# Kernel tuning notes

Measured on AMD Instinct MI355X. Metric: run time of the kernel, lower is better.

Reference implementation:

```python
import jax, jax.numpy as jnp
import numpy as np

N = 50000
IN, HID, OUT, HEADS = 128, 64, 64, 4


def seg_softmax(logits, seg, num):
    # softmax over edges grouped by destination node; logits [E, H]
    m = jax.ops.segment_max(logits, seg, num_segments=num)
    e = jnp.exp(logits - m[seg])
    s = jax.ops.segment_sum(e, seg, num_segments=num)
    return e / (s[seg] + 1e-16)


def gat_conv(x, src, dst, W, a_s, a_d, b, heads, concat):
    n = x.shape[0]
    h = (x @ W.T).reshape(n, heads, -1)           # [N, H, C]
    alpha_src = jnp.einsum('nhc,hc->nh', h, a_s)   # per-node src score
    alpha_dst = jnp.einsum('nhc,hc->nh', h, a_d)
    logits = jax.nn.leaky_relu(alpha_src[src] + alpha_dst[dst], 0.2)  # [E, H]
    alpha = seg_softmax(logits, dst, n)
    out = jax.ops.segment_sum(alpha[:, :, None] * h[src], dst, num_segments=n)  # [N, H, C]
    out = out.reshape(n, -1) if concat else out.mean(axis=1)
    return out + b


def setup_inputs():
    key = jax.random.key(0)
    ks = jax.random.split(key, 16)
    x = jax.random.normal(ks[0], (N, IN), dtype=jnp.float32)
    edge_index = jax.random.randint(ks[1], (2, 800000), 0, N, dtype=jnp.int64)

    def glorot(k, shape):
        fan = shape[-1]
        return jax.random.normal(k, shape, dtype=jnp.float32) / jnp.sqrt(jnp.float32(fan))

    d = {"x": x, "edge_index": edge_index}
    # layer 1: IN -> HID, HEADS heads, concat
    d["W1"] = glorot(ks[2], (HEADS * HID, IN))
    d["as1"] = glorot(ks[3], (HEADS, HID))
    d["ad1"] = glorot(ks[4], (HEADS, HID))
    d["b1"] = jnp.zeros((HEADS * HID,), jnp.float32)
    # layer 2: HID*HEADS -> HID, HEADS heads, concat
    d["W2"] = glorot(ks[5], (HEADS * HID, HEADS * HID))
    d["as2"] = glorot(ks[6], (HEADS, HID))
    d["ad2"] = glorot(ks[7], (HEADS, HID))
    d["b2"] = jnp.zeros((HEADS * HID,), jnp.float32)
    # layer 3: HID*HEADS -> OUT, 1 head
    d["W3"] = glorot(ks[8], (OUT, HEADS * HID))
    d["as3"] = glorot(ks[9], (1, OUT))
    d["ad3"] = glorot(ks[10], (1, OUT))
    d["b3"] = jnp.zeros((OUT,), jnp.float32)
    return d


def reference(x, edge_index, W1, as1, ad1, b1, W2, as2, ad2, b2, W3, as3, ad3, b3):
    # PyG GATConv adds self-loops by default
    loops = jnp.arange(N, dtype=edge_index.dtype)
    src = jnp.concatenate([edge_index[0], loops])
    dst = jnp.concatenate([edge_index[1], loops])

    h = jax.nn.relu(gat_conv(x, src, dst, W1, as1, ad1, b1, HEADS, True))
    h = jax.nn.relu(gat_conv(h, src, dst, W2, as2, ad2, b2, HEADS, True))
    out = gat_conv(h, src, dst, W3, as3, ad3, b3, 1, True)
    return out
```

## Files before the change

### kernel.cpp

```cpp
#include <hip/hip_runtime.h>
#include <hip/hip_bf16.h>
#include <math.h>


typedef __bf16 bf16x8 __attribute__((ext_vector_type(8)));
typedef float f32x4 __attribute__((ext_vector_type(4)));

#define QINV 2048.0f
#define QDQ  4.8828125e-4f

__device__ __forceinline__ void gload_lds16(const void* g, void* l) {
  __builtin_amdgcn_global_load_lds(
      (const __attribute__((address_space(1))) unsigned int*)g,
      (__attribute__((address_space(3))) unsigned int*)l, 16, 0, 0);
}

__device__ __forceinline__ unsigned int splitf(float a) {
  __hip_bfloat16 h = __float2bfloat16(a);
  float hf = __bfloat162float(h);
  __hip_bfloat16 l = __float2bfloat16(a - hf);
  return (unsigned int)__builtin_bit_cast(unsigned short, h) |
         ((unsigned int)__builtin_bit_cast(unsigned short, l) << 16);
}

__device__ __forceinline__ float leaky02(float l) {
  return (l >= 0.f) ? l : 0.2f * l;
}

__device__ __forceinline__ short quant16(float v) {
  int q = (int)rintf(v * QINV);
  q = q > 32767 ? 32767 : (q < -32768 ? -32768 : q);
  return (short)q;
}


__global__ void init_counts_kernel(int* counts, int n) {
  int i = blockIdx.x * blockDim.x + threadIdx.x;
  if (i < n) counts[i] = 1;
}

__global__ void hist_kernel(const int* __restrict__ dst, int e, int* counts) {
  int i = blockIdx.x * blockDim.x + threadIdx.x;
  if (i < e) atomicAdd(&counts[dst[i]], 1);
}

__global__ __launch_bounds__(1024) void block_sum_kernel(const int* __restrict__ counts,
                                                         int* __restrict__ bsum, int n) {
  __shared__ int red[1024];
  int i = blockIdx.x * 1024 + threadIdx.x;
  red[threadIdx.x] = (i < n) ? counts[i] : 0;
  __syncthreads();
  #pragma unroll
  for (int off = 512; off > 0; off >>= 1) {
    if (threadIdx.x < off) red[threadIdx.x] += red[threadIdx.x + off];
    __syncthreads();
  }
  if (threadIdx.x == 0) bsum[blockIdx.x] = red[0];
}

__global__ void scan_sums_kernel(int* bsum, int nb) {
  int t = threadIdx.x;
  int c = (t < nb) ? bsum[t] : 0;
  int v = c;
  #pragma unroll
  for (int off = 1; off < 64; off <<= 1) {
    int u = __shfl_up(v, off);
    if (t >= off) v += u;
  }
  if (t < nb) bsum[t] = v - c;
}

__global__ __launch_bounds__(1024) void scan_final_kernel(const int* __restrict__ counts,
    const int* __restrict__ bsum, int* __restrict__ offsets, int* __restrict__ cursor, int n) {
  __shared__ int sc[1024];
  int i = blockIdx.x * 1024 + threadIdx.x;
  int c = (i < n) ? counts[i] : 0;
  sc[threadIdx.x] = c;
  __syncthreads();
  for (int off = 1; off < 1024; off <<= 1) {
    int v = 0;
    if (threadIdx.x >= off) v = sc[threadIdx.x - off];
    __syncthreads();
    sc[threadIdx.x] += v;
    __syncthreads();
  }
  int excl = sc[threadIdx.x] - c + bsum[blockIdx.x];
  if (i < n) {
    offsets[i] = excl;
    cursor[i] = excl;
  } else if (i == n) {
    offsets[n] = excl;
  }
}

__global__ void scatter_kernel(const int* __restrict__ src, const int* __restrict__ dst,
                               int e800, int etot, int* cursor, int* __restrict__ ssrc) {
  int i = blockIdx.x * blockDim.x + threadIdx.x;
  if (i >= etot) return;
  int s, d;
  if (i < e800) { s = src[i]; d = dst[i]; }
  else          { s = i - e800; d = s; }
  int pos = atomicAdd(&cursor[d], 1);
  ssrc[pos] = s;
}

__global__ void split_kernel(const float* __restrict__ in, uint4* __restrict__ out, int count4) {
  int i = blockIdx.x * blockDim.x + threadIdx.x;
  if (i >= count4) return;
  float4 v = reinterpret_cast<const float4*>(in)[i];
  uint4 o;
  o.x = splitf(v.x); o.y = splitf(v.y); o.z = splitf(v.z); o.w = splitf(v.w);
  out[i] = o;
}

template <int KP, int BN, int WAVES_M, int WAVES_N>
__global__ __launch_bounds__(256) void gemm2_kernel(
    const unsigned short* __restrict__ A, const unsigned short* __restrict__ B,
    short* __restrict__ Cq, int M) {
  constexpr int BM = 64, BK = 64;
  constexpr int NK = KP / BK;
  constexpr int MFRAG = BM / WAVES_M / 16;
  constexpr int NFRAG = BN / WAVES_N / 16;
  __shared__ unsigned short As[2][BM * BK];
  __shared__ unsigned short Bs[2][BN * BK];

  const int tid = threadIdx.x;
  const int lane = tid & 63;
  const int wid = tid >> 6;
  const int m0 = blockIdx.x * BM;

  const int srow = tid >> 3;
  const int scolb = (tid & 7) * 16;
  const int sswz = (srow & 7) << 4;
  const char* aSrc = (const char*)A + (size_t)(m0 + srow) * (KP * 2) + (scolb ^ sswz);
  const char* bSrc = (const char*)B + (size_t)srow * (KP * 2) + (scolb ^ sswz);
  char* aDst0 = (char*)&As[0][0] + wid * 1024;
  char* bDst0 = (char*)&Bs[0][0] + wid * 1024;

  auto stage = [&](int buf, int kt) {
    const size_t ko = (size_t)kt * 128;
    char* ad = aDst0 + buf * (BM * 128);
    #pragma unroll
    for (int i = 0; i < BM / 32; ++i)
      gload_lds16(aSrc + ko + (size_t)i * 32 * (KP * 2), ad + i * 4096);
    char* bd = bDst0 + buf * (BN * 128);
    #pragma unroll
    for (int j = 0; j < BN / 32; ++j)
      gload_lds16(bSrc + ko + (size_t)j * 32 * (KP * 2), bd + j * 4096);
  };

  const int fr = lane & 15;
  const int fg = lane >> 4;
  const int fswz = (fr & 7) << 4;
  const int wm0 = (WAVES_M > 1) ? wid * (BM / WAVES_M) : 0;
  const int wn0 = (WAVES_N > 1) ? wid * (BN / WAVES_N) : 0;

  f32x4 acc[MFRAG][NFRAG];
  #pragma unroll
  for (int mi = 0; mi < MFRAG; ++mi)
    #pragma unroll
    for (int ni = 0; ni < NFRAG; ++ni) acc[mi][ni] = (f32x4)0.f;

  stage(0, 0);
  __syncthreads();

  for (int kt = 0; kt < NK; ++kt) {
    const int buf = kt & 1;
    if (kt + 1 < NK) stage(buf ^ 1, kt + 1);
    const char* asB = (const char*)&As[buf][0] + (wm0 + fr) * 128;
    const char* bsB = (const char*)&Bs[buf][0] + (wn0 + fr) * 128;
    #pragma unroll
    for (int kh = 0; kh < 2; ++kh) {
      const int kb = (kh * 64 + fg * 16) ^ fswz;
      bf16x8 af[MFRAG], bfr[NFRAG];
      #pragma unroll
      for (int mi = 0; mi < MFRAG; ++mi)
        af[mi] = *reinterpret_cast<const bf16x8*>(asB + mi * 16 * 128 + kb);
      #pragma unroll
      for (int ni = 0; ni < NFRAG; ++ni)
        bfr[ni] = *reinterpret_cast<const bf16x8*>(bsB + ni * 16 * 128 + kb);
      #pragma unroll
      for (int mi = 0; mi < MFRAG; ++mi)
        #pragma unroll
        for (int ni = 0; ni < NFRAG; ++ni)
          acc[mi][ni] = __builtin_amdgcn_mfma_f32_16x16x32_bf16(af[mi], bfr[ni], acc[mi][ni], 0, 0, 0);
    }
    __syncthreads();
  }

  #pragma unroll
  for (int mi = 0; mi < MFRAG; ++mi) {
    #pragma unroll
    for (int r = 0; r < 4; ++r) {
      int row = m0 + wm0 + mi * 16 + fg * 4 + r;
      if (row < M) {
        #pragma unroll
        for (int ni = 0; ni < NFRAG; ++ni)
          Cq[(size_t)row * BN + wn0 + ni * 16 + fr] = quant16(acc[mi][ni][r]);
      }
    }
  }
}

__global__ __launch_bounds__(256) void alpha4_kernel(const short* __restrict__ hq,
    const float* __restrict__ a_s, const float* __restrict__ a_d,
    float* __restrict__ asrc, float* __restrict__ adst, int n) {
  int wid = threadIdx.x >> 6;
  int lane = threadIdx.x & 63;
  int node = blockIdx.x * 4 + wid;
  if (node >= n) return;
  short4 q = *reinterpret_cast<const short4*>(&hq[(size_t)node * 256 + lane * 4]);
  float4 sv = *reinterpret_cast<const float4*>(&a_s[lane * 4]);
  float4 dv = *reinterpret_cast<const float4*>(&a_d[lane * 4]);
  float h0 = (float)q.x, h1 = (float)q.y, h2 = (float)q.z, h3 = (float)q.w;
  float ps = h0 * sv.x + h1 * sv.y + h2 * sv.z + h3 * sv.w;
  float pd = h0 * dv.x + h1 * dv.y + h2 * dv.z + h3 * dv.w;
  #pragma unroll
  for (int off = 1; off < 16; off <<= 1) {
    ps += __shfl_xor(ps, off);
    pd += __shfl_xor(pd, off);
  }
  if ((lane & 15) == 0) {
    int head = lane >> 4;
    asrc[node * 4 + head] = ps * QDQ;
    adst[node * 4 + head] = pd * QDQ;
  }
}

__global__ __launch_bounds__(256) void alpha1_kernel(const short* __restrict__ hq,
    const float* __restrict__ a_s, const float* __restrict__ a_d,
    float* __restrict__ asrc, float* __restrict__ adst, int n) {
  int wid = threadIdx.x >> 6;
  int lane = threadIdx.x & 63;
  int node = blockIdx.x * 4 + wid;
  if (node >= n) return;
  float hv = (float)hq[(size_t)node * 64 + lane];
  float ps = hv * a_s[lane];
  float pd = hv * a_d[lane];
  #pragma unroll
  for (int off = 1; off < 64; off <<= 1) {
    ps += __shfl_xor(ps, off);
    pd += __shfl_xor(pd, off);
  }
  if (lane == 0) { asrc[node] = ps * QDQ; adst[node] = pd * QDQ; }
}

template <bool RELU, bool SPLIT>
__global__ __launch_bounds__(256) void aggregate4_kernel(
    const short* __restrict__ hq, const float* __restrict__ asrc,
    const float* __restrict__ adst, const float* __restrict__ bias,
    const int* __restrict__ offsets, const int* __restrict__ ssrc,
    void* __restrict__ outp, int n) {
  int wid = threadIdx.x >> 6;
  int lane = threadIdx.x & 63;
  int node = blockIdx.x * 4 + wid;
  if (node >= n) return;
  int head = lane >> 4;
  float adv = adst[(size_t)node * 4 + head];
  int beg = offsets[node], end = offsets[node + 1];

  float m0 = -INFINITY, m1 = -INFINITY, m2 = -INFINITY, m3 = -INFINITY;
  int e = beg;
  for (; e + 3 < end; e += 4) {
    float l0 = leaky02(asrc[(size_t)ssrc[e + 0] * 4 + head] + adv);
    float l1 = leaky02(asrc[(size_t)ssrc[e + 1] * 4 + head] + adv);
    float l2 = leaky02(asrc[(size_t)ssrc[e + 2] * 4 + head] + adv);
    float l3 = leaky02(asrc[(size_t)ssrc[e + 3] * 4 + head] + adv);
    m0 = fmaxf(m0, l0); m1 = fmaxf(m1, l1);
    m2 = fmaxf(m2, l2); m3 = fmaxf(m3, l3);
  }
  for (; e < end; ++e)
    m0 = fmaxf(m0, leaky02(asrc[(size_t)ssrc[e] * 4 + head] + adv));
  const float m = fmaxf(fmaxf(m0, m1), fmaxf(m2, m3));

  float s0 = 0.f, s1 = 0.f, s2 = 0.f, s3 = 0.f;
  float4 A0 = {0, 0, 0, 0}, A1 = {0, 0, 0, 0}, A2 = {0, 0, 0, 0}, A3 = {0, 0, 0, 0};
  e = beg;
  for (; e + 3 < end; e += 4) {
    int c0 = ssrc[e + 0], c1 = ssrc[e + 1], c2 = ssrc[e + 2], c3 = ssrc[e + 3];
    float p0 = __expf(leaky02(asrc[(size_t)c0 * 4 + head] + adv) - m);
    float p1 = __expf(leaky02(asrc[(size_t)c1 * 4 + head] + adv) - m);
    float p2 = __expf(leaky02(asrc[(size_t)c2 * 4 + head] + adv) - m);
    float p3 = __expf(leaky02(asrc[(size_t)c3 * 4 + head] + adv) - m);
    short4 q0 = *reinterpret_cast<const short4*>(&hq[(size_t)c0 * 256 + lane * 4]);
    short4 q1 = *reinterpret_cast<const short4*>(&hq[(size_t)c1 * 256 + lane * 4]);
    short4 q2 = *reinterpret_cast<const short4*>(&hq[(size_t)c2 * 256 + lane * 4]);
    short4 q3 = *reinterpret_cast<const short4*>(&hq[(size_t)c3 * 256 + lane * 4]);
    s0 += p0; s1 += p1; s2 += p2; s3 += p3;
    A0.x += p0 * (float)q0.x; A0.y += p0 * (float)q0.y; A0.z += p0 * (float)q0.z; A0.w += p0 * (float)q0.w;
    A1.x += p1 * (float)q1.x; A1.y += p1 * (float)q1.y; A1.z += p1 * (float)q1.z; A1.w += p1 * (float)q1.w;
    A2.x += p2 * (float)q2.x; A2.y += p2 * (float)q2.y; A2.z += p2 * (float)q2.z; A2.w += p2 * (float)q2.w;
    A3.x += p3 * (float)q3.x; A3.y += p3 * (float)q3.y; A3.z += p3 * (float)q3.z; A3.w += p3 * (float)q3.w;
  }
  for (; e < end; ++e) {
    int c0 = ssrc[e];
    float p0 = __expf(leaky02(asrc[(size_t)c0 * 4 + head] + adv) - m);
    short4 q0 = *reinterpret_cast<const short4*>(&hq[(size_t)c0 * 256 + lane * 4]);
    s0 += p0;
    A0.x += p0 * (float)q0.x; A0.y += p0 * (float)q0.y; A0.z += p0 * (float)q0.z; A0.w += p0 * (float)q0.w;
  }
  float s = (s0 + s1) + (s2 + s3);
  float4 A;
  A.x = (A0.x + A1.x) + (A2.x + A3.x);
  A.y = (A0.y + A1.y) + (A2.y + A3.y);
  A.z = (A0.z + A1.z) + (A2.z + A3.z);
  A.w = (A0.w + A1.w) + (A2.w + A3.w);

  float inv = QDQ / (s + 1e-16f);
  float4 bv = *reinterpret_cast<const float4*>(&bias[lane * 4]);
  float4 o;
  o.x = A.x * inv + bv.x;
  o.y = A.y * inv + bv.y;
  o.z = A.z * inv + bv.z;
  o.w = A.w * inv + bv.w;
  if (RELU) {
    o.x = fmaxf(o.x, 0.f); o.y = fmaxf(o.y, 0.f);
    o.z = fmaxf(o.z, 0.f); o.w = fmaxf(o.w, 0.f);
  }
  if (SPLIT) {
    uint4 pk;
    pk.x = splitf(o.x); pk.y = splitf(o.y); pk.z = splitf(o.z); pk.w = splitf(o.w);
    reinterpret_cast<uint4*>(outp)[(size_t)node * 64 + lane] = pk;
  } else {
    reinterpret_cast<float4*>(outp)[(size_t)node * 64 + lane] = o;
  }
}

__global__ __launch_bounds__(256) void aggregate1_kernel(
    const short* __restrict__ hq, const float* __restrict__ asrc,
    const float* __restrict__ adst, const float* __restrict__ bias,
    const int* __restrict__ offsets, const int* __restrict__ ssrc,
    float* __restrict__ out, int n) {
  int wid = threadIdx.x >> 6;
  int lane = threadIdx.x & 63;
  int node = blockIdx.x * 4 + wid;
  if (node >= n) return;
  int g = lane >> 4;
  int w = lane & 15;
  float adv = adst[node];
  int beg = offsets[node], end = offsets[node + 1];

  float m = -INFINITY;
  for (int e = beg + lane; e < end; e += 64)
    m = fmaxf(m, leaky02(asrc[ssrc[e]] + adv));
  #pragma unroll
  for (int off = 1; off < 64; off <<= 1) m = fmaxf(m, __shfl_xor(m, off));

  float s = 0.f;
  float4 A = {0, 0, 0, 0};
  int e0 = beg;
  for (; e0 + 3 < end; e0 += 4) {
    int src = ssrc[e0 + g];
    float p = __expf(leaky02(asrc[src] + adv) - m);
    short4 q = *reinterpret_cast<const short4*>(&hq[(size_t)src * 64 + w * 4]);
    s += p;
    A.x += p * (float)q.x; A.y += p * (float)q.y;
    A.z += p * (float)q.z; A.w += p * (float)q.w;
  }
  if (e0 + g < end) {
    int src = ssrc[e0 + g];
    float p = __expf(leaky02(asrc[src] + adv) - m);
    short4 q = *reinterpret_cast<const short4*>(&hq[(size_t)src * 64 + w * 4]);
    s += p;
    A.x += p * (float)q.x; A.y += p * (float)q.y;
    A.z += p * (float)q.z; A.w += p * (float)q.w;
  }
  #pragma unroll
  for (int off = 16; off < 64; off <<= 1) {
    s += __shfl_xor(s, off);
    A.x += __shfl_xor(A.x, off);
    A.y += __shfl_xor(A.y, off);
    A.z += __shfl_xor(A.z, off);
    A.w += __shfl_xor(A.w, off);
  }
  if (g == 0) {
    float inv = QDQ / (s + 1e-16f);
    float4 bv = *reinterpret_cast<const float4*>(&bias[w * 4]);
    float4 o;
    o.x = A.x * inv + bv.x;
    o.y = A.y * inv + bv.y;
    o.z = A.z * inv + bv.z;
    o.w = A.w * inv + bv.w;
    *reinterpret_cast<float4*>(&out[(size_t)node * 64 + w * 4]) = o;
  }
}


extern "C" void kernel_launch(void* const* d_in, const int* in_sizes, int n_in,
                              void* d_out, int out_size, void* d_ws, size_t ws_size,
                              hipStream_t stream) {
  const float* x   = (const float*)d_in[0];
  const int*   ei  = (const int*)d_in[1];
  const float* W1  = (const float*)d_in[2];
  const float* as1 = (const float*)d_in[3];
  const float* ad1 = (const float*)d_in[4];
  const float* b1  = (const float*)d_in[5];
  const float* W2  = (const float*)d_in[6];
  const float* as2 = (const float*)d_in[7];
  const float* ad2 = (const float*)d_in[8];
  const float* b2  = (const float*)d_in[9];
  const float* W3  = (const float*)d_in[10];
  const float* as3 = (const float*)d_in[11];
  const float* ad3 = (const float*)d_in[12];
  const float* b3  = (const float*)d_in[13];
  float* out = (float*)d_out;

  const int n    = in_sizes[0] / 128;
  const int e800 = in_sizes[1] / 2;
  const int etot = e800 + n;
  const int Mpad = 50048;

  char* ws = (char*)d_ws;
  size_t off = 0;
  auto alloc = [&](size_t bytes) -> void* {
    void* p = ws + off;
    off = (off + bytes + 255) & ~(size_t)255;
    return p;
  };
  short*          featQ  = (short*)alloc((size_t)Mpad * 256 * 2);
  unsigned short* hsplit = (unsigned short*)alloc((size_t)Mpad * 512 * 2);
  unsigned short* w1s    = (unsigned short*)alloc((size_t)256 * 256 * 2);
  unsigned short* w2s    = (unsigned short*)alloc((size_t)256 * 512 * 2);
  unsigned short* w3s    = (unsigned short*)alloc((size_t)64 * 512 * 2);
  float* asrc    = (float*)alloc((size_t)n * 4 * 4);
  float* adst    = (float*)alloc((size_t)n * 4 * 4);
  int*   ssrc    = (int*)alloc((size_t)etot * 4);
  int*   offsets = (int*)alloc((size_t)(n + 1) * 4);
  int*   cursor  = (int*)alloc((size_t)n * 4);
  int*   counts  = (int*)alloc((size_t)n * 4);
  int*   bsum    = (int*)alloc((size_t)64 * 4);

  const int* esrc = ei;
  const int* edst = ei + e800;
  const int nbScan = (n + 1024) / 1024;

  init_counts_kernel<<<(n + 255) / 256, 256, 0, stream>>>(counts, n);
  hist_kernel<<<(e800 + 255) / 256, 256, 0, stream>>>(edst, e800, counts);
  block_sum_kernel<<<nbScan, 1024, 0, stream>>>(counts, bsum, n);
  scan_sums_kernel<<<1, 64, 0, stream>>>(bsum, nbScan);
  scan_final_kernel<<<nbScan, 1024, 0, stream>>>(counts, bsum, offsets, cursor, n);
  scatter_kernel<<<(etot + 255) / 256, 256, 0, stream>>>(esrc, edst, e800, etot, cursor, ssrc);

  split_kernel<<<(n * 128 / 4 + 255) / 256, 256, 0, stream>>>(x, (uint4*)hsplit, n * 128 / 4);
  split_kernel<<<(256 * 128 / 4 + 255) / 256, 256, 0, stream>>>(W1, (uint4*)w1s, 256 * 128 / 4);
  split_kernel<<<(256 * 256 / 4 + 255) / 256, 256, 0, stream>>>(W2, (uint4*)w2s, 256 * 256 / 4);
  split_kernel<<<(64 * 256 / 4 + 255) / 256, 256, 0, stream>>>(W3, (uint4*)w3s, 64 * 256 / 4);

  const int nodeBlocks = (n + 3) / 4;
  const int mBlocks = Mpad / 64;

  gemm2_kernel<256, 256, 1, 4><<<mBlocks, 256, 0, stream>>>(hsplit, w1s, featQ, n);
  alpha4_kernel<<<nodeBlocks, 256, 0, stream>>>(featQ, as1, ad1, asrc, adst, n);
  aggregate4_kernel<true, true><<<nodeBlocks, 256, 0, stream>>>(featQ, asrc, adst, b1, offsets, ssrc, hsplit, n);

  gemm2_kernel<512, 256, 1, 4><<<mBlocks, 256, 0, stream>>>(hsplit, w2s, featQ, n);
  alpha4_kernel<<<nodeBlocks, 256, 0, stream>>>(featQ, as2, ad2, asrc, adst, n);
  aggregate4_kernel<true, true><<<nodeBlocks, 256, 0, stream>>>(featQ, asrc, adst, b2, offsets, ssrc, hsplit, n);

  gemm2_kernel<512, 64, 4, 1><<<mBlocks, 256, 0, stream>>>(hsplit, w3s, featQ, n);
  alpha1_kernel<<<nodeBlocks, 256, 0, stream>>>(featQ, as3, ad3, asrc, adst, n);
  aggregate1_kernel<<<nodeBlocks, 256, 0, stream>>>(featQ, asrc, adst, b3, offsets, ssrc, out, n);
}
```

Baseline: 400.6 us.

## Retile GEMM into 2D 128x128 blocks and drop softmax max pass

```diff
diff --git a/kernel.cpp b/kernel.cpp
--- a/kernel.cpp
+++ b/kernel.cpp
@@ -113,11 +113,11 @@
   out[i] = o;
 }
 
-template <int KP, int BN, int WAVES_M, int WAVES_N>
+template <int KP, int BM, int BN, int WAVES_M, int WAVES_N, int OTOT>
 __global__ __launch_bounds__(256) void gemm2_kernel(
     const unsigned short* __restrict__ A, const unsigned short* __restrict__ B,
     short* __restrict__ Cq, int M) {
-  constexpr int BM = 64, BK = 64;
+  constexpr int BK = 64;
   constexpr int NK = KP / BK;
   constexpr int MFRAG = BM / WAVES_M / 16;
   constexpr int NFRAG = BN / WAVES_N / 16;
@@ -128,12 +128,13 @@
   const int lane = tid & 63;
   const int wid = tid >> 6;
   const int m0 = blockIdx.x * BM;
+  const int o0 = blockIdx.y * BN;
 
   const int srow = tid >> 3;
   const int scolb = (tid & 7) * 16;
   const int sswz = (srow & 7) << 4;
   const char* aSrc = (const char*)A + (size_t)(m0 + srow) * (KP * 2) + (scolb ^ sswz);
-  const char* bSrc = (const char*)B + (size_t)srow * (KP * 2) + (scolb ^ sswz);
+  const char* bSrc = (const char*)B + (size_t)(o0 + srow) * (KP * 2) + (scolb ^ sswz);
   char* aDst0 = (char*)&As[0][0] + wid * 1024;
   char* bDst0 = (char*)&Bs[0][0] + wid * 1024;
 
@@ -152,8 +153,8 @@
   const int fr = lane & 15;
   const int fg = lane >> 4;
   const int fswz = (fr & 7) << 4;
-  const int wm0 = (WAVES_M > 1) ? wid * (BM / WAVES_M) : 0;
-  const int wn0 = (WAVES_N > 1) ? wid * (BN / WAVES_N) : 0;
+  const int wm0 = (wid / WAVES_N) * (BM / WAVES_M);
+  const int wn0 = (wid % WAVES_N) * (BN / WAVES_N);
 
   f32x4 acc[MFRAG][NFRAG];
   #pragma unroll
@@ -196,7 +197,7 @@
       if (row < M) {
         #pragma unroll
         for (int ni = 0; ni < NFRAG; ++ni)
-          Cq[(size_t)row * BN + wn0 + ni * 16 + fr] = quant16(acc[mi][ni][r]);
+          Cq[(size_t)row * OTOT + o0 + wn0 + ni * 16 + fr] = quant16(acc[mi][ni][r]);
       }
     }
   }
@@ -259,29 +260,15 @@
   float adv = adst[(size_t)node * 4 + head];
   int beg = offsets[node], end = offsets[node + 1];
 
-  float m0 = -INFINITY, m1 = -INFINITY, m2 = -INFINITY, m3 = -INFINITY;
+  float s0 = 0.f, s1 = 0.f, s2 = 0.f, s3 = 0.f;
+  float4 A0 = {0, 0, 0, 0}, A1 = {0, 0, 0, 0}, A2 = {0, 0, 0, 0}, A3 = {0, 0, 0, 0};
   int e = beg;
   for (; e + 3 < end; e += 4) {
-    float l0 = leaky02(asrc[(size_t)ssrc[e + 0] * 4 + head] + adv);
-    float l1 = leaky02(asrc[(size_t)ssrc[e + 1] * 4 + head] + adv);
-    float l2 = leaky02(asrc[(size_t)ssrc[e + 2] * 4 + head] + adv);
-    float l3 = leaky02(asrc[(size_t)ssrc[e + 3] * 4 + head] + adv);
-    m0 = fmaxf(m0, l0); m1 = fmaxf(m1, l1);
-    m2 = fmaxf(m2, l2); m3 = fmaxf(m3, l3);
-  }
-  for (; e < end; ++e)
-    m0 = fmaxf(m0, leaky02(asrc[(size_t)ssrc[e] * 4 + head] + adv));
-  const float m = fmaxf(fmaxf(m0, m1), fmaxf(m2, m3));
-
-  float s0 = 0.f, s1 = 0.f, s2 = 0.f, s3 = 0.f;
-  float4 A0 = {0, 0, 0, 0}, A1 = {0, 0, 0, 0}, A2 = {0, 0, 0, 0}, A3 = {0, 0, 0, 0};
-  e = beg;
-  for (; e + 3 < end; e += 4) {
     int c0 = ssrc[e + 0], c1 = ssrc[e + 1], c2 = ssrc[e + 2], c3 = ssrc[e + 3];
-    float p0 = __expf(leaky02(asrc[(size_t)c0 * 4 + head] + adv) - m);
-    float p1 = __expf(leaky02(asrc[(size_t)c1 * 4 + head] + adv) - m);
-    float p2 = __expf(leaky02(asrc[(size_t)c2 * 4 + head] + adv) - m);
-    float p3 = __expf(leaky02(asrc[(size_t)c3 * 4 + head] + adv) - m);
+    float p0 = __expf(leaky02(asrc[(size_t)c0 * 4 + head] + adv));
+    float p1 = __expf(leaky02(asrc[(size_t)c1 * 4 + head] + adv));
+    float p2 = __expf(leaky02(asrc[(size_t)c2 * 4 + head] + adv));
+    float p3 = __expf(leaky02(asrc[(size_t)c3 * 4 + head] + adv));
     short4 q0 = *reinterpret_cast<const short4*>(&hq[(size_t)c0 * 256 + lane * 4]);
     short4 q1 = *reinterpret_cast<const short4*>(&hq[(size_t)c1 * 256 + lane * 4]);
     short4 q2 = *reinterpret_cast<const short4*>(&hq[(size_t)c2 * 256 + lane * 4]);
@@ -294,7 +281,7 @@
   }
   for (; e < end; ++e) {
     int c0 = ssrc[e];
-    float p0 = __expf(leaky02(asrc[(size_t)c0 * 4 + head] + adv) - m);
+    float p0 = __expf(leaky02(asrc[(size_t)c0 * 4 + head] + adv));
     short4 q0 = *reinterpret_cast<const short4*>(&hq[(size_t)c0 * 256 + lane * 4]);
     s0 += p0;
     A0.x += p0 * (float)q0.x; A0.y += p0 * (float)q0.y; A0.z += p0 * (float)q0.z; A0.w += p0 * (float)q0.w;
@@ -340,18 +327,12 @@
   float adv = adst[node];
   int beg = offsets[node], end = offsets[node + 1];
 
-  float m = -INFINITY;
-  for (int e = beg + lane; e < end; e += 64)
-    m = fmaxf(m, leaky02(asrc[ssrc[e]] + adv));
-  #pragma unroll
-  for (int off = 1; off < 64; off <<= 1) m = fmaxf(m, __shfl_xor(m, off));
-
   float s = 0.f;
   float4 A = {0, 0, 0, 0};
   int e0 = beg;
   for (; e0 + 3 < end; e0 += 4) {
     int src = ssrc[e0 + g];
-    float p = __expf(leaky02(asrc[src] + adv) - m);
+    float p = __expf(leaky02(asrc[src] + adv));
     short4 q = *reinterpret_cast<const short4*>(&hq[(size_t)src * 64 + w * 4]);
     s += p;
     A.x += p * (float)q.x; A.y += p * (float)q.y;
@@ -359,7 +340,7 @@
   }
   if (e0 + g < end) {
     int src = ssrc[e0 + g];
-    float p = __expf(leaky02(asrc[src] + adv) - m);
+    float p = __expf(leaky02(asrc[src] + adv));
     short4 q = *reinterpret_cast<const short4*>(&hq[(size_t)src * 64 + w * 4]);
     s += p;
     A.x += p * (float)q.x; A.y += p * (float)q.y;
@@ -447,17 +428,17 @@
   split_kernel<<<(64 * 256 / 4 + 255) / 256, 256, 0, stream>>>(W3, (uint4*)w3s, 64 * 256 / 4);
 
   const int nodeBlocks = (n + 3) / 4;
-  const int mBlocks = Mpad / 64;
-
-  gemm2_kernel<256, 256, 1, 4><<<mBlocks, 256, 0, stream>>>(hsplit, w1s, featQ, n);
+  const int mBlocks = Mpad / 128;
+
+  gemm2_kernel<256, 128, 128, 2, 2, 256><<<dim3(mBlocks, 2), 256, 0, stream>>>(hsplit, w1s, featQ, n);
   alpha4_kernel<<<nodeBlocks, 256, 0, stream>>>(featQ, as1, ad1, asrc, adst, n);
   aggregate4_kernel<true, true><<<nodeBlocks, 256, 0, stream>>>(featQ, asrc, adst, b1, offsets, ssrc, hsplit, n);
 
-  gemm2_kernel<512, 256, 1, 4><<<mBlocks, 256, 0, stream>>>(hsplit, w2s, featQ, n);
+  gemm2_kernel<512, 128, 128, 2, 2, 256><<<dim3(mBlocks, 2), 256, 0, stream>>>(hsplit, w2s, featQ, n);
   alpha4_kernel<<<nodeBlocks, 256, 0, stream>>>(featQ, as2, ad2, asrc, adst, n);
   aggregate4_kernel<true, true><<<nodeBlocks, 256, 0, stream>>>(featQ, asrc, adst, b2, offsets, ssrc, hsplit, n);
 
-  gemm2_kernel<512, 64, 4, 1><<<mBlocks, 256, 0, stream>>>(hsplit, w3s, featQ, n);
+  gemm2_kernel<512, 128, 64, 4, 1, 64><<<dim3(mBlocks, 1), 256, 0, stream>>>(hsplit, w3s, featQ, n);
   alpha1_kernel<<<nodeBlocks, 256, 0, stream>>>(featQ, as3, ad3, asrc, adst, n);
   aggregate1_kernel<<<nodeBlocks, 256, 0, stream>>>(featQ, asrc, adst, b3, offsets, ssrc, out, n);
 }
```

Result: faster. 373.2 us (-6.8%).
